# Performance work log

Hardware: AMD Instinct MI355X
Metric: run time of the kernel (lower is better)

Reference implementation:

```python
import jax, jax.numpy as jnp
import numpy as np

HIDDEN = 128
NUM_HEADS = 8
F32_MIN = jnp.finfo(jnp.float32).min


def _split_heads(x, n):
    # [B, S, D] -> [B, n, S, D//n]
    b, s, d = x.shape
    return x.reshape(b, s, n, d // n).transpose(0, 2, 1, 3)


def setup_inputs() -> dict:
    key = jax.random.key(0)
    k1, k2, k3 = jax.random.split(key, 3)
    B, S = 4, 2048
    key_and_value = jax.random.normal(k1, (B, S, 2 * HIDDEN), dtype=jnp.float32)
    query = jax.random.normal(k2, (B, S, HIDDEN), dtype=jnp.float32)
    seq_len = jax.random.randint(k3, (B, 1), 1, S + 1, dtype=jnp.int32)
    return {"key_and_value": key_and_value, "query": query, "seq_len": seq_len}


def reference(key_and_value, query, seq_len):
    B, S, _ = query.shape
    d_head = HIDDEN // NUM_HEADS
    k, v = jnp.split(key_and_value, 2, axis=2)           # each [B, S, HIDDEN]
    Q = _split_heads(query, NUM_HEADS) * (d_head ** 0.5)  # NOTE: original MULTIPLIES by sqrt(d_head)
    K = _split_heads(k, NUM_HEADS)
    V = _split_heads(v, NUM_HEADS)
    # scores: [B, H, S, S]
    logits = jnp.einsum('bhqd,bhkd->bhqk', Q, K)
    # length mask over key positions: valid where pos < seq_len (one-hot+cumsum trick)
    valid = (jnp.arange(S, dtype=jnp.int32)[None, :] < seq_len).astype(jnp.float32)  # [B, S]
    logits = logits + F32_MIN * (1.0 - valid[:, None, None, :])
    weights = jax.nn.softmax(logits, axis=-1)
    out = jnp.einsum('bhqk,bhkd->bhqd', weights, V)       # [B, H, S, d_head]
    return out.transpose(0, 2, 1, 3).reshape(B, S, HIDDEN)
```

## Files before the change

### kernel.cpp

```cpp
#include <hip/hip_runtime.h>
#include <hip/hip_bf16.h>

#define HIDDEN 128
#define NHEAD  8
#define DHEAD  16
#define KBLK   64
#define QPB    2
#define TILEB  6144
#define QSCALE 5.77078016355585277626f

typedef __attribute__((ext_vector_type(8))) __bf16 bf16x8;
typedef __attribute__((ext_vector_type(4))) __bf16 bf16x4;
typedef __attribute__((ext_vector_type(4))) float  f32x4;
typedef __attribute__((ext_vector_type(2))) float  f32x2;
typedef __attribute__((ext_vector_type(4))) int    i32x4;

__device__ __forceinline__ int ksub(int k)  { return ((k >> 5) << 1) | ((k >> 2) & 1); }
__device__ __forceinline__ int kirow(int k) { return (((k >> 3) & 3) << 2) | (k & 3); }

__device__ __forceinline__ void cvt_store(char* Sb, int ka, i32x4 vaddr,
                                          f32x4 kvec, f32x4 vvec)
{
    bf16x4 khv, klv;
    #pragma unroll
    for (int i = 0; i < 4; ++i) {
        __bf16 hi = (__bf16)kvec[i];
        khv[i] = hi;
        klv[i] = (__bf16)(kvec[i] - (float)hi);
    }
    *(bf16x4*)(Sb + ka)        = khv;
    *(bf16x4*)(Sb + 2048 + ka) = klv;
    #pragma unroll
    for (int i = 0; i < 4; ++i)
        *(__bf16*)(Sb + vaddr[i]) = (__bf16)vvec[i];
}

template<bool SPLIT>
__global__ __launch_bounds__(256, 4)
void mha_fwd(const float* __restrict__ kv,
             const float* __restrict__ q,
             const int*   __restrict__ seq_len,
             float* __restrict__ out,
             float* __restrict__ pbuf,
             float* __restrict__ mlbuf,
             int S, int nc, int chunk)
{
    const int qpair = blockIdx.x;
    const int h     = blockIdx.y;
    int b, c0;
    if (SPLIT) { const int Bn = gridDim.z / nc; b = blockIdx.z % Bn; c0 = blockIdx.z / Bn; }
    else       { b = blockIdx.z; c0 = 0; }
    const int L = seq_len[b];
    const int kstart = SPLIT ? c0 * chunk : 0;
    if (SPLIT && kstart >= L) return;
    const int kend = SPLIT ? min(L, kstart + chunk) : L;

    const int tid  = threadIdx.x;
    const int lane = tid & 63;
    const int wave = tid >> 6;
    const int g    = lane >> 4;
    const int lr   = lane & 15;
    const int sw   = (lr & 7) << 4;

    __shared__ __align__(16) char Stg[2][TILEB];

    const int qrowb = qpair * (QPB * KBLK) + wave * 16 + lr;
    bf16x8 qf[QPB];
    #pragma unroll
    for (int qt = 0; qt < QPB; ++qt) {
        const float* qp = q + ((size_t)(b * S + qrowb + qt * KBLK) * HIDDEN) + h * DHEAD + (g & 1) * 8;
        #pragma unroll
        for (int j = 0; j < 8; ++j) {
            float qv = qp[j] * QSCALE;
            __bf16 hi = (__bf16)qv;
            qf[qt][j] = (g < 2) ? hi : (__bf16)(qv - (float)hi);
        }
    }

    const int sk = tid >> 2;
    const int qd = tid & 3;
    const float* kvp = kv + ((size_t)(b * S + sk) * (2 * HIDDEN)) + h * DHEAD + 4 * qd;
    const int ka = ksub(sk) * 512 + (qd >> 1) * 256 + kirow(sk) * 16 + (qd & 1) * 8;
    i32x4 vaddr;
    #pragma unroll
    for (int i = 0; i < 4; ++i) {
        const int d = 4 * qd + i;
        vaddr[i] = 4096 + d * 128 + (((sk >> 3) * 16) ^ ((d & 7) << 4)) + (sk & 7) * 2;
    }

    f32x4 acc[QPB];
    float m[QPB], lsum[QPB];
    #pragma unroll
    for (int qt = 0; qt < QPB; ++qt) {
        acc[qt] = (f32x4){0.f, 0.f, 0.f, 0.f};
        m[qt] = -1e30f; lsum[qt] = 0.f;
    }

    const int ntiles = (kend - kstart + KBLK - 1) >> 6;

    {
        const float* kp = kvp + (size_t)kstart * (2 * HIDDEN);
        f32x4 kvec = *(const f32x4*)kp;
        f32x4 vvec = *(const f32x4*)(kp + HIDDEN);
        cvt_store(&Stg[0][0], ka, vaddr, kvec, vvec);
    }
    __syncthreads();

    for (int ti = 0; ti < ntiles; ++ti) {
        const int kb = kstart + ti * KBLK;
        const char* Sb = &Stg[ti & 1][0];
        const bool hasnext = (ti + 1) < ntiles;

        f32x4 nkv, nvv;
        if (hasnext) {
            const float* kp = kvp + (size_t)(kb + KBLK) * (2 * HIDDEN);
            nkv = *(const f32x4*)kp;
            nvv = *(const f32x4*)(kp + HIDDEN);
        }

        bf16x8 kfh[4], kfl[4];
        #pragma unroll
        for (int sub = 0; sub < 4; ++sub) {
            kfh[sub] = *(const bf16x8*)(Sb + sub * 512 + (g & 1) * 256 + lr * 16);
            kfl[sub] = *(const bf16x8*)(Sb + 2048 + sub * 512 + (g & 1) * 256 + lr * 16);
        }
        bf16x8 vb0 = *(const bf16x8*)(Sb + 4096 + lr * 128 + ((g * 16) ^ sw));
        bf16x8 vb1 = *(const bf16x8*)(Sb + 4096 + lr * 128 + ((64 + g * 16) ^ sw));

        const bool bnd = (kb + KBLK > kend);

        #pragma unroll
        for (int qt = 0; qt < QPB; ++qt) {
            f32x4 s[4];
            #pragma unroll
            for (int sub = 0; sub < 4; ++sub) {
                f32x4 z = {0.f, 0.f, 0.f, 0.f};
                z = __builtin_amdgcn_mfma_f32_16x16x32_bf16(kfh[sub], qf[qt], z, 0, 0, 0);
                s[sub] = __builtin_amdgcn_mfma_f32_16x16x32_bf16(kfl[sub], qf[qt], z, 0, 0, 0);
            }
            if (bnd) {
                #pragma unroll
                for (int sub = 0; sub < 4; ++sub) {
                    const int kb2 = kb + (sub >> 1) * 32 + (sub & 1) * 4 + g * 8;
                    #pragma unroll
                    for (int r = 0; r < 4; ++r)
                        if (kb2 + r >= kend) s[sub][r] = -1e30f;
                }
            }

            float t0 = fmaxf(fmaxf(s[0][0], s[0][1]), fmaxf(s[0][2], s[0][3]));
            float t1 = fmaxf(fmaxf(s[1][0], s[1][1]), fmaxf(s[1][2], s[1][3]));
            float t2 = fmaxf(fmaxf(s[2][0], s[2][1]), fmaxf(s[2][2], s[2][3]));
            float t3 = fmaxf(fmaxf(s[3][0], s[3][1]), fmaxf(s[3][2], s[3][3]));
            float tmax = fmaxf(fmaxf(t0, t1), fmaxf(t2, t3));
            tmax = fmaxf(tmax, __shfl_xor(tmax, 16));
            tmax = fmaxf(tmax, __shfl_xor(tmax, 32));

            const float mn = fmaxf(m[qt], tmax);
            const float alpha = exp2f(m[qt] - mn);
            m[qt] = mn;

            float rsum = 0.f;
            bf16x8 pa0, pa1;
            #pragma unroll
            for (int sub = 0; sub < 2; ++sub)
                #pragma unroll
                for (int r = 0; r < 4; ++r) {
                    float p = exp2f(s[sub][r] - mn);
                    rsum += p;
                    pa0[sub * 4 + r] = (__bf16)p;
                }
            #pragma unroll
            for (int sub = 2; sub < 4; ++sub)
                #pragma unroll
                for (int r = 0; r < 4; ++r) {
                    float p = exp2f(s[sub][r] - mn);
                    rsum += p;
                    pa1[(sub - 2) * 4 + r] = (__bf16)p;
                }
            rsum += __shfl_xor(rsum, 16);
            rsum += __shfl_xor(rsum, 32);
            lsum[qt] = lsum[qt] * alpha + rsum;
            acc[qt] *= alpha;

            acc[qt] = __builtin_amdgcn_mfma_f32_16x16x32_bf16(vb0, pa0, acc[qt], 0, 0, 0);
            acc[qt] = __builtin_amdgcn_mfma_f32_16x16x32_bf16(vb1, pa1, acc[qt], 0, 0, 0);
        }

        if (hasnext)
            cvt_store(&Stg[(ti + 1) & 1][0], ka, vaddr, nkv, nvv);
        __syncthreads();
    }

    #pragma unroll
    for (int qt = 0; qt < QPB; ++qt) {
        const int qglob = qrowb + qt * KBLK;
        if (SPLIT) {
            const size_t row = (((size_t)b * nc + c0) * S + qglob) * NHEAD + h;
            *(f32x4*)&pbuf[row * DHEAD + g * 4] = acc[qt];
            if (g == 0) { f32x2 ml = {m[qt], lsum[qt]}; *(f32x2*)&mlbuf[row * 2] = ml; }
        } else {
            const float inv = 1.0f / lsum[qt];
            *(f32x4*)&out[((size_t)b * S + qglob) * HIDDEN + h * DHEAD + g * 4] = acc[qt] * inv;
        }
    }
}

__global__ __launch_bounds__(256)
void mha_merge(const float* __restrict__ pbuf, const float* __restrict__ mlbuf,
               const int* __restrict__ seq_len, float* __restrict__ out,
               int S, int nc, int chunk)
{
    const int t = blockIdx.x * 256 + threadIdx.x;
    const int h = t & (NHEAD - 1);
    const int rest = t >> 3;
    const int qg = rest % S;
    const int b  = rest / S;
    const int L  = seq_len[b];
    const int nch = min(nc, (L + chunk - 1) / chunk);

    const size_t cstr = (size_t)S * NHEAD;
    const size_t row0 = ((size_t)b * nc) * cstr + (size_t)qg * NHEAD + h;

    float mv[8], lv[8];
    float M = -1e30f;
    for (int c = 0; c < nch; ++c) {
        f32x2 ml = *(const f32x2*)&mlbuf[(row0 + c * cstr) * 2];
        mv[c] = ml[0]; lv[c] = ml[1];
        M = fmaxf(M, ml[0]);
    }
    float den = 0.f;
    f32x4 o0 = {0,0,0,0}, o1 = o0, o2 = o0, o3 = o0;
    for (int c = 0; c < nch; ++c) {
        float w = exp2f(mv[c] - M);
        den += w * lv[c];
        const float* pp = &pbuf[(row0 + c * cstr) * DHEAD];
        o0 += w * *(const f32x4*)&pp[0];
        o1 += w * *(const f32x4*)&pp[4];
        o2 += w * *(const f32x4*)&pp[8];
        o3 += w * *(const f32x4*)&pp[12];
    }
    const float inv = 1.0f / den;
    float* op = &out[((size_t)b * S + qg) * HIDDEN + h * DHEAD];
    *(f32x4*)&op[0]  = o0 * inv;
    *(f32x4*)&op[4]  = o1 * inv;
    *(f32x4*)&op[8]  = o2 * inv;
    *(f32x4*)&op[12] = o3 * inv;
}

extern "C" void kernel_launch(void* const* d_in, const int* in_sizes, int n_in,
                              void* d_out, int out_size, void* d_ws, size_t ws_size,
                              hipStream_t stream)
{
    const float* kv      = (const float*)d_in[0];
    const float* query   = (const float*)d_in[1];
    const int*   seq_len = (const int*)d_in[2];
    float* out           = (float*)d_out;

    const int B = in_sizes[2];
    const int S = in_sizes[1] / (B * HIDDEN);

    int chunk = 0, nc = 1;
    size_t pb = 0, mlb = 0;
    for (int cand = 256; cand <= 512; cand <<= 1) {
        int n = (S + cand - 1) / cand;
        size_t pbc  = (size_t)B * n * S * NHEAD * DHEAD * sizeof(float);
        size_t mlbc = (size_t)B * n * S * NHEAD * 2 * sizeof(float);
        if (n <= 8 && ws_size >= pbc + mlbc) { chunk = cand; nc = n; pb = pbc; mlb = mlbc; break; }
    }

    if (chunk) {
        float* pbuf  = (float*)d_ws;
        float* mlbuf = (float*)((char*)d_ws + pb);
        mha_fwd<true><<<dim3(S / (QPB * KBLK), NHEAD, B * nc), dim3(256), 0, stream>>>(
            kv, query, seq_len, nullptr, pbuf, mlbuf, S, nc, chunk);
        const int nrows = B * S * NHEAD;
        mha_merge<<<dim3((nrows + 255) / 256), dim3(256), 0, stream>>>(
            pbuf, mlbuf, seq_len, out, S, nc, chunk);
    } else {
        mha_fwd<false><<<dim3(S / (QPB * KBLK), NHEAD, B), dim3(256), 0, stream>>>(
            kv, query, seq_len, out, nullptr, nullptr, S, 1, S);
    }
}
```

Baseline: 47.27 us.

## Use persistent atomic work queue for split-K attention and store partials as bf16

Replaces the fixed 3D grid with a persistent kernel of up to 2048 blocks that pull (q-pair, head, batch, chunk) work items from a global atomic counter. The counter is zeroed with a memset each call. Items whose chunk lies past seq_len are skipped cheaply rather than occupying a whole block launch, which targets load imbalance from the variable sequence lengths. Partial output accumulators are written as bf16 instead of fp32 to cut workspace traffic into the merge kernel, at some cost in precision. The change also adds an extra memset launch and a per-item atomic plus barrier.

```diff
diff --git a/kernel.cpp b/kernel.cpp
--- a/kernel.cpp
+++ b/kernel.cpp
@@ -41,45 +41,24 @@
              const float* __restrict__ q,
              const int*   __restrict__ seq_len,
              float* __restrict__ out,
-             float* __restrict__ pbuf,
+             __hip_bfloat16* __restrict__ pbuf,
              float* __restrict__ mlbuf,
-             int S, int nc, int chunk)
+             int* __restrict__ wq,
+             int S, int nb, int nc, int chunk, int nitems)
 {
-    const int qpair = blockIdx.x;
-    const int h     = blockIdx.y;
-    int b, c0;
-    if (SPLIT) { const int Bn = gridDim.z / nc; b = blockIdx.z % Bn; c0 = blockIdx.z / Bn; }
-    else       { b = blockIdx.z; c0 = 0; }
-    const int L = seq_len[b];
-    const int kstart = SPLIT ? c0 * chunk : 0;
-    if (SPLIT && kstart >= L) return;
-    const int kend = SPLIT ? min(L, kstart + chunk) : L;
-
     const int tid  = threadIdx.x;
     const int lane = tid & 63;
     const int wave = tid >> 6;
     const int g    = lane >> 4;
     const int lr   = lane & 15;
     const int sw   = (lr & 7) << 4;
+    const int QP   = S / (QPB * KBLK);
 
     __shared__ __align__(16) char Stg[2][TILEB];
-
-    const int qrowb = qpair * (QPB * KBLK) + wave * 16 + lr;
-    bf16x8 qf[QPB];
-    #pragma unroll
-    for (int qt = 0; qt < QPB; ++qt) {
-        const float* qp = q + ((size_t)(b * S + qrowb + qt * KBLK) * HIDDEN) + h * DHEAD + (g & 1) * 8;
-        #pragma unroll
-        for (int j = 0; j < 8; ++j) {
-            float qv = qp[j] * QSCALE;
-            __bf16 hi = (__bf16)qv;
-            qf[qt][j] = (g < 2) ? hi : (__bf16)(qv - (float)hi);
-        }
-    }
+    __shared__ int s_item;
 
     const int sk = tid >> 2;
     const int qd = tid & 3;
-    const float* kvp = kv + ((size_t)(b * S + sk) * (2 * HIDDEN)) + h * DHEAD + 4 * qd;
     const int ka = ksub(sk) * 512 + (qd >> 1) * 256 + kirow(sk) * 16 + (qd & 1) * 8;
     i32x4 vaddr;
     #pragma unroll
@@ -88,126 +67,169 @@
         vaddr[i] = 4096 + d * 128 + (((sk >> 3) * 16) ^ ((d & 7) << 4)) + (sk & 7) * 2;
     }
 
-    f32x4 acc[QPB];
-    float m[QPB], lsum[QPB];
-    #pragma unroll
-    for (int qt = 0; qt < QPB; ++qt) {
-        acc[qt] = (f32x4){0.f, 0.f, 0.f, 0.f};
-        m[qt] = -1e30f; lsum[qt] = 0.f;
-    }
-
-    const int ntiles = (kend - kstart + KBLK - 1) >> 6;
-
-    {
-        const float* kp = kvp + (size_t)kstart * (2 * HIDDEN);
-        f32x4 kvec = *(const f32x4*)kp;
-        f32x4 vvec = *(const f32x4*)(kp + HIDDEN);
-        cvt_store(&Stg[0][0], ka, vaddr, kvec, vvec);
-    }
-    __syncthreads();
-
-    for (int ti = 0; ti < ntiles; ++ti) {
-        const int kb = kstart + ti * KBLK;
-        const char* Sb = &Stg[ti & 1][0];
-        const bool hasnext = (ti + 1) < ntiles;
-
-        f32x4 nkv, nvv;
-        if (hasnext) {
-            const float* kp = kvp + (size_t)(kb + KBLK) * (2 * HIDDEN);
-            nkv = *(const f32x4*)kp;
-            nvv = *(const f32x4*)(kp + HIDDEN);
-        }
-
-        bf16x8 kfh[4], kfl[4];
-        #pragma unroll
-        for (int sub = 0; sub < 4; ++sub) {
-            kfh[sub] = *(const bf16x8*)(Sb + sub * 512 + (g & 1) * 256 + lr * 16);
-            kfl[sub] = *(const bf16x8*)(Sb + 2048 + sub * 512 + (g & 1) * 256 + lr * 16);
-        }
-        bf16x8 vb0 = *(const bf16x8*)(Sb + 4096 + lr * 128 + ((g * 16) ^ sw));
-        bf16x8 vb1 = *(const bf16x8*)(Sb + 4096 + lr * 128 + ((64 + g * 16) ^ sw));
-
-        const bool bnd = (kb + KBLK > kend);
-
+    for (int it = blockIdx.x; ; it += gridDim.x) {
+        int item;
+        if (wq) {
+            if (tid == 0) s_item = atomicAdd(wq, 1);
+            __syncthreads();
+            item = s_item;
+        } else {
+            item = it;
+        }
+        if (item >= nitems) return;
+
+        const int qp = item % QP;
+        int t1 = item / QP;
+        const int h  = t1 % NHEAD;
+        int t2 = t1 / NHEAD;
+        const int b  = t2 % nb;
+        const int c0 = t2 / nb;
+
+        const int L = seq_len[b];
+        const int kstart = SPLIT ? c0 * chunk : 0;
+        if (SPLIT && kstart >= L) { if (!wq) return; else continue; }
+        const int kend = SPLIT ? min(L, kstart + chunk) : L;
+
+        const int qrowb = qp * (QPB * KBLK) + wave * 16 + lr;
+        bf16x8 qf[QPB];
         #pragma unroll
         for (int qt = 0; qt < QPB; ++qt) {
-            f32x4 s[4];
+            const float* qpp = q + ((size_t)(b * S + qrowb + qt * KBLK) * HIDDEN) + h * DHEAD + (g & 1) * 8;
+            #pragma unroll
+            for (int j = 0; j < 8; ++j) {
+                float qv = qpp[j] * QSCALE;
+                __bf16 hi = (__bf16)qv;
+                qf[qt][j] = (g < 2) ? hi : (__bf16)(qv - (float)hi);
+            }
+        }
+
+        const float* kvp = kv + ((size_t)(b * S + sk) * (2 * HIDDEN)) + h * DHEAD + 4 * qd;
+
+        f32x4 acc[QPB];
+        float m[QPB], lsum[QPB];
+        #pragma unroll
+        for (int qt = 0; qt < QPB; ++qt) {
+            acc[qt] = (f32x4){0.f, 0.f, 0.f, 0.f};
+            m[qt] = -1e30f; lsum[qt] = 0.f;
+        }
+
+        const int ntiles = (kend - kstart + KBLK - 1) >> 6;
+
+        {
+            const float* kp = kvp + (size_t)kstart * (2 * HIDDEN);
+            f32x4 kvec = *(const f32x4*)kp;
+            f32x4 vvec = *(const f32x4*)(kp + HIDDEN);
+            cvt_store(&Stg[0][0], ka, vaddr, kvec, vvec);
+        }
+        __syncthreads();
+
+        for (int ti = 0; ti < ntiles; ++ti) {
+            const int kb = kstart + ti * KBLK;
+            const char* Sb = &Stg[ti & 1][0];
+            const bool hasnext = (ti + 1) < ntiles;
+
+            f32x4 nkv, nvv;
+            if (hasnext) {
+                const float* kp = kvp + (size_t)(kb + KBLK) * (2 * HIDDEN);
+                nkv = *(const f32x4*)kp;
+                nvv = *(const f32x4*)(kp + HIDDEN);
+            }
+
+            bf16x8 kfh[4], kfl[4];
             #pragma unroll
             for (int sub = 0; sub < 4; ++sub) {
-                f32x4 z = {0.f, 0.f, 0.f, 0.f};
-                z = __builtin_amdgcn_mfma_f32_16x16x32_bf16(kfh[sub], qf[qt], z, 0, 0, 0);
-                s[sub] = __builtin_amdgcn_mfma_f32_16x16x32_bf16(kfl[sub], qf[qt], z, 0, 0, 0);
-            }
-            if (bnd) {
+                kfh[sub] = *(const bf16x8*)(Sb + sub * 512 + (g & 1) * 256 + lr * 16);
+                kfl[sub] = *(const bf16x8*)(Sb + 2048 + sub * 512 + (g & 1) * 256 + lr * 16);
+            }
+            bf16x8 vb0 = *(const bf16x8*)(Sb + 4096 + lr * 128 + ((g * 16) ^ sw));
+            bf16x8 vb1 = *(const bf16x8*)(Sb + 4096 + lr * 128 + ((64 + g * 16) ^ sw));
+
+            const bool bnd = (kb + KBLK > kend);
+
+            #pragma unroll
+            for (int qt = 0; qt < QPB; ++qt) {
+                f32x4 s[4];
                 #pragma unroll
                 for (int sub = 0; sub < 4; ++sub) {
-                    const int kb2 = kb + (sub >> 1) * 32 + (sub & 1) * 4 + g * 8;
+                    f32x4 z = {0.f, 0.f, 0.f, 0.f};
+                    z = __builtin_amdgcn_mfma_f32_16x16x32_bf16(kfh[sub], qf[qt], z, 0, 0, 0);
+                    s[sub] = __builtin_amdgcn_mfma_f32_16x16x32_bf16(kfl[sub], qf[qt], z, 0, 0, 0);
+                }
+                if (bnd) {
                     #pragma unroll
-                    for (int r = 0; r < 4; ++r)
-                        if (kb2 + r >= kend) s[sub][r] = -1e30f;
+                    for (int sub = 0; sub < 4; ++sub) {
+                        const int kb2 = kb + (sub >> 1) * 32 + (sub & 1) * 4 + g * 8;
+                        #pragma unroll
+                        for (int r = 0; r < 4; ++r)
+                            if (kb2 + r >= kend) s[sub][r] = -1e30f;
+                    }
                 }
-            }
-
-            float t0 = fmaxf(fmaxf(s[0][0], s[0][1]), fmaxf(s[0][2], s[0][3]));
-            float t1 = fmaxf(fmaxf(s[1][0], s[1][1]), fmaxf(s[1][2], s[1][3]));
-            float t2 = fmaxf(fmaxf(s[2][0], s[2][1]), fmaxf(s[2][2], s[2][3]));
-            float t3 = fmaxf(fmaxf(s[3][0], s[3][1]), fmaxf(s[3][2], s[3][3]));
-            float tmax = fmaxf(fmaxf(t0, t1), fmaxf(t2, t3));
-            tmax = fmaxf(tmax, __shfl_xor(tmax, 16));
-            tmax = fmaxf(tmax, __shfl_xor(tmax, 32));
-
-            const float mn = fmaxf(m[qt], tmax);
-            const float alpha = exp2f(m[qt] - mn);
-            m[qt] = mn;
-
-            float rsum = 0.f;
-            bf16x8 pa0, pa1;
-            #pragma unroll
-            for (int sub = 0; sub < 2; ++sub)
+
+                float t0 = fmaxf(fmaxf(s[0][0], s[0][1]), fmaxf(s[0][2], s[0][3]));
+                float t1v = fmaxf(fmaxf(s[1][0], s[1][1]), fmaxf(s[1][2], s[1][3]));
+                float t2v = fmaxf(fmaxf(s[2][0], s[2][1]), fmaxf(s[2][2], s[2][3]));
+                float t3v = fmaxf(fmaxf(s[3][0], s[3][1]), fmaxf(s[3][2], s[3][3]));
+                float tmax = fmaxf(fmaxf(t0, t1v), fmaxf(t2v, t3v));
+                tmax = fmaxf(tmax, __shfl_xor(tmax, 16));
+                tmax = fmaxf(tmax, __shfl_xor(tmax, 32));
+
+                const float mn = fmaxf(m[qt], tmax);
+                const float alpha = exp2f(m[qt] - mn);
+                m[qt] = mn;
+
+                float rsum = 0.f;
+                bf16x8 pa0, pa1;
                 #pragma unroll
-                for (int r = 0; r < 4; ++r) {
-                    float p = exp2f(s[sub][r] - mn);
-                    rsum += p;
-                    pa0[sub * 4 + r] = (__bf16)p;
-                }
-            #pragma unroll
-            for (int sub = 2; sub < 4; ++sub)
+                for (int sub = 0; sub < 2; ++sub)
+                    #pragma unroll
+                    for (int r = 0; r < 4; ++r) {
+                        float p = exp2f(s[sub][r] - mn);
+                        rsum += p;
+                        pa0[sub * 4 + r] = (__bf16)p;
+                    }
                 #pragma unroll
-                for (int r = 0; r < 4; ++r) {
-                    float p = exp2f(s[sub][r] - mn);
-                    rsum += p;
-                    pa1[(sub - 2) * 4 + r] = (__bf16)p;
-                }
-            rsum += __shfl_xor(rsum, 16);
-            rsum += __shfl_xor(rsum, 32);
-            lsum[qt] = lsum[qt] * alpha + rsum;
-            acc[qt] *= alpha;
-
-            acc[qt] = __builtin_amdgcn_mfma_f32_16x16x32_bf16(vb0, pa0, acc[qt], 0, 0, 0);
-            acc[qt] = __builtin_amdgcn_mfma_f32_16x16x32_bf16(vb1, pa1, acc[qt], 0, 0, 0);
-        }
-
-        if (hasnext)
-            cvt_store(&Stg[(ti + 1) & 1][0], ka, vaddr, nkv, nvv);
-        __syncthreads();
-    }
-
-    #pragma unroll
-    for (int qt = 0; qt < QPB; ++qt) {
-        const int qglob = qrowb + qt * KBLK;
-        if (SPLIT) {
-            const size_t row = (((size_t)b * nc + c0) * S + qglob) * NHEAD + h;
-            *(f32x4*)&pbuf[row * DHEAD + g * 4] = acc[qt];
-            if (g == 0) { f32x2 ml = {m[qt], lsum[qt]}; *(f32x2*)&mlbuf[row * 2] = ml; }
-        } else {
-            const float inv = 1.0f / lsum[qt];
-            *(f32x4*)&out[((size_t)b * S + qglob) * HIDDEN + h * DHEAD + g * 4] = acc[qt] * inv;
-        }
+                for (int sub = 2; sub < 4; ++sub)
+                    #pragma unroll
+                    for (int r = 0; r < 4; ++r) {
+                        float p = exp2f(s[sub][r] - mn);
+                        rsum += p;
+                        pa1[(sub - 2) * 4 + r] = (__bf16)p;
+                    }
+                rsum += __shfl_xor(rsum, 16);
+                rsum += __shfl_xor(rsum, 32);
+                lsum[qt] = lsum[qt] * alpha + rsum;
+                acc[qt] *= alpha;
+
+                acc[qt] = __builtin_amdgcn_mfma_f32_16x16x32_bf16(vb0, pa0, acc[qt], 0, 0, 0);
+                acc[qt] = __builtin_amdgcn_mfma_f32_16x16x32_bf16(vb1, pa1, acc[qt], 0, 0, 0);
+            }
+
+            if (hasnext)
+                cvt_store(&Stg[(ti + 1) & 1][0], ka, vaddr, nkv, nvv);
+            __syncthreads();
+        }
+
+        #pragma unroll
+        for (int qt = 0; qt < QPB; ++qt) {
+            const int qglob = qrowb + qt * KBLK;
+            if (SPLIT) {
+                const size_t row = (((size_t)b * nc + c0) * S + qglob) * NHEAD + h;
+                bf16x4 pk;
+                #pragma unroll
+                for (int r = 0; r < 4; ++r) pk[r] = (__bf16)acc[qt][r];
+                *(bf16x4*)&pbuf[row * DHEAD + g * 4] = pk;
+                if (g == 0) { f32x2 ml = {m[qt], lsum[qt]}; *(f32x2*)&mlbuf[row * 2] = ml; }
+            } else {
+                const float inv = 1.0f / lsum[qt];
+                *(f32x4*)&out[((size_t)b * S + qglob) * HIDDEN + h * DHEAD + g * 4] = acc[qt] * inv;
+            }
+        }
+        if (!wq) { if (it + gridDim.x >= nitems) return; }
     }
 }
 
 __global__ __launch_bounds__(256)
-void mha_merge(const float* __restrict__ pbuf, const float* __restrict__ mlbuf,
+void mha_merge(const __hip_bfloat16* __restrict__ pbuf, const float* __restrict__ mlbuf,
                const int* __restrict__ seq_len, float* __restrict__ out,
                int S, int nc, int chunk)
 {
@@ -230,22 +252,28 @@
         M = fmaxf(M, ml[0]);
     }
     float den = 0.f;
-    f32x4 o0 = {0,0,0,0}, o1 = o0, o2 = o0, o3 = o0;
+    float o[16];
+    #pragma unroll
+    for (int i = 0; i < 16; ++i) o[i] = 0.f;
     for (int c = 0; c < nch; ++c) {
         float w = exp2f(mv[c] - M);
         den += w * lv[c];
-        const float* pp = &pbuf[(row0 + c * cstr) * DHEAD];
-        o0 += w * *(const f32x4*)&pp[0];
-        o1 += w * *(const f32x4*)&pp[4];
-        o2 += w * *(const f32x4*)&pp[8];
-        o3 += w * *(const f32x4*)&pp[12];
+        const __hip_bfloat16* pp = &pbuf[(row0 + c * cstr) * DHEAD];
+        bf16x8 p0 = *(const bf16x8*)&pp[0];
+        bf16x8 p1 = *(const bf16x8*)&pp[8];
+        #pragma unroll
+        for (int i = 0; i < 8; ++i) {
+            o[i]     += w * (float)p0[i];
+            o[i + 8] += w * (float)p1[i];
+        }
     }
     const float inv = 1.0f / den;
     float* op = &out[((size_t)b * S + qg) * HIDDEN + h * DHEAD];
-    *(f32x4*)&op[0]  = o0 * inv;
-    *(f32x4*)&op[4]  = o1 * inv;
-    *(f32x4*)&op[8]  = o2 * inv;
-    *(f32x4*)&op[12] = o3 * inv;
+    #pragma unroll
+    for (int i = 0; i < 4; ++i) {
+        f32x4 v = {o[4*i] * inv, o[4*i+1] * inv, o[4*i+2] * inv, o[4*i+3] * inv};
+        *(f32x4*)&op[4 * i] = v;
+    }
 }
 
 extern "C" void kernel_launch(void* const* d_in, const int* in_sizes, int n_in,
@@ -259,26 +287,32 @@
 
     const int B = in_sizes[2];
     const int S = in_sizes[1] / (B * HIDDEN);
+    const int QP = S / (QPB * KBLK);
 
     int chunk = 0, nc = 1;
-    size_t pb = 0, mlb = 0;
-    for (int cand = 256; cand <= 512; cand <<= 1) {
+    size_t mlb = 0, pbb = 0;
+    for (int cand = 256; cand <= S; cand <<= 1) {
         int n = (S + cand - 1) / cand;
-        size_t pbc  = (size_t)B * n * S * NHEAD * DHEAD * sizeof(float);
         size_t mlbc = (size_t)B * n * S * NHEAD * 2 * sizeof(float);
-        if (n <= 8 && ws_size >= pbc + mlbc) { chunk = cand; nc = n; pb = pbc; mlb = mlbc; break; }
+        size_t pbbc = (size_t)B * n * S * NHEAD * DHEAD * sizeof(__hip_bfloat16);
+        if (n <= 8 && ws_size >= 64 + mlbc + pbbc) { chunk = cand; nc = n; mlb = mlbc; pbb = pbbc; break; }
     }
 
     if (chunk) {
-        float* pbuf  = (float*)d_ws;
-        float* mlbuf = (float*)((char*)d_ws + pb);
-        mha_fwd<true><<<dim3(S / (QPB * KBLK), NHEAD, B * nc), dim3(256), 0, stream>>>(
-            kv, query, seq_len, nullptr, pbuf, mlbuf, S, nc, chunk);
+        int* wq = (int*)d_ws;
+        float* mlbuf = (float*)((char*)d_ws + 64);
+        __hip_bfloat16* pbuf = (__hip_bfloat16*)((char*)d_ws + 64 + mlb);
+        hipMemsetAsync(d_ws, 0, 64, stream);
+        const int nitems = nc * B * NHEAD * QP;
+        const int grid = nitems < 2048 ? nitems : 2048;
+        mha_fwd<true><<<dim3(grid), dim3(256), 0, stream>>>(
+            kv, query, seq_len, nullptr, pbuf, mlbuf, wq, S, B, nc, chunk, nitems);
         const int nrows = B * S * NHEAD;
         mha_merge<<<dim3((nrows + 255) / 256), dim3(256), 0, stream>>>(
             pbuf, mlbuf, seq_len, out, S, nc, chunk);
     } else {
-        mha_fwd<false><<<dim3(S / (QPB * KBLK), NHEAD, B), dim3(256), 0, stream>>>(
-            kv, query, seq_len, out, nullptr, nullptr, S, 1, S);
+        const int nitems = B * NHEAD * QP;
+        mha_fwd<false><<<dim3(nitems), dim3(256), 0, stream>>>(
+            kv, query, seq_len, out, nullptr, nullptr, nullptr, S, B, 1, S, nitems);
     }
 }
```

Measured after the change: 98.00 us. 2.07x slower.

## Switch attention to fp16 MFMA, drop K hi/lo split, fp16 partials

Applied to the files above, without the earlier changes.

Replaces the bf16 hi/lo split of K (two MFMAs per score tile) with a single fp16 MFMA, halving QK MFMA count and shrinking the shared-memory K tile. V and P also move to fp16. Split-K partial outputs are stored as fp16 to halve workspace traffic, and the chunk size is fixed at 512, giving fewer chunks and a cheaper merge. This trades accuracy: K and the partial accumulators lose the extra precision, and fp16 range is narrower than bf16, though the scaled softmax probabilities stay bounded in [0,1].

```diff
diff --git a/kernel.cpp b/kernel.cpp
--- a/kernel.cpp
+++ b/kernel.cpp
@@ -6,11 +6,11 @@
 #define DHEAD  16
 #define KBLK   64
 #define QPB    2
-#define TILEB  6144
+#define TILEB  4096
 #define QSCALE 5.77078016355585277626f
 
-typedef __attribute__((ext_vector_type(8))) __bf16 bf16x8;
-typedef __attribute__((ext_vector_type(4))) __bf16 bf16x4;
+typedef __attribute__((ext_vector_type(8))) _Float16 f16x8;
+typedef __attribute__((ext_vector_type(4))) _Float16 f16x4;
 typedef __attribute__((ext_vector_type(4))) float  f32x4;
 typedef __attribute__((ext_vector_type(2))) float  f32x2;
 typedef __attribute__((ext_vector_type(4))) int    i32x4;
@@ -21,18 +21,13 @@
 __device__ __forceinline__ void cvt_store(char* Sb, int ka, i32x4 vaddr,
                                           f32x4 kvec, f32x4 vvec)
 {
-    bf16x4 khv, klv;
-    #pragma unroll
-    for (int i = 0; i < 4; ++i) {
-        __bf16 hi = (__bf16)kvec[i];
-        khv[i] = hi;
-        klv[i] = (__bf16)(kvec[i] - (float)hi);
-    }
-    *(bf16x4*)(Sb + ka)        = khv;
-    *(bf16x4*)(Sb + 2048 + ka) = klv;
+    f16x4 kh;
+    #pragma unroll
+    for (int i = 0; i < 4; ++i) kh[i] = (_Float16)kvec[i];
+    *(f16x4*)(Sb + ka) = kh;
     #pragma unroll
     for (int i = 0; i < 4; ++i)
-        *(__bf16*)(Sb + vaddr[i]) = (__bf16)vvec[i];
+        *(_Float16*)(Sb + vaddr[i]) = (_Float16)vvec[i];
 }
 
 template<bool SPLIT>
@@ -41,7 +36,7 @@
              const float* __restrict__ q,
              const int*   __restrict__ seq_len,
              float* __restrict__ out,
-             float* __restrict__ pbuf,
+             _Float16* __restrict__ pbuf,
              float* __restrict__ mlbuf,
              int S, int nc, int chunk)
 {
@@ -65,15 +60,15 @@
     __shared__ __align__(16) char Stg[2][TILEB];
 
     const int qrowb = qpair * (QPB * KBLK) + wave * 16 + lr;
-    bf16x8 qf[QPB];
+    f16x8 qf[QPB];
     #pragma unroll
     for (int qt = 0; qt < QPB; ++qt) {
         const float* qp = q + ((size_t)(b * S + qrowb + qt * KBLK) * HIDDEN) + h * DHEAD + (g & 1) * 8;
         #pragma unroll
         for (int j = 0; j < 8; ++j) {
             float qv = qp[j] * QSCALE;
-            __bf16 hi = (__bf16)qv;
-            qf[qt][j] = (g < 2) ? hi : (__bf16)(qv - (float)hi);
+            _Float16 hi = (_Float16)qv;
+            qf[qt][j] = (g < 2) ? hi : (_Float16)(qv - (float)hi);
         }
     }
 
@@ -85,7 +80,7 @@
     #pragma unroll
     for (int i = 0; i < 4; ++i) {
         const int d = 4 * qd + i;
-        vaddr[i] = 4096 + d * 128 + (((sk >> 3) * 16) ^ ((d & 7) << 4)) + (sk & 7) * 2;
+        vaddr[i] = 2048 + d * 128 + (((sk >> 3) * 16) ^ ((d & 7) << 4)) + (sk & 7) * 2;
     }
 
     f32x4 acc[QPB];
@@ -118,14 +113,12 @@
             nvv = *(const f32x4*)(kp + HIDDEN);
         }
 
-        bf16x8 kfh[4], kfl[4];
-        #pragma unroll
-        for (int sub = 0; sub < 4; ++sub) {
-            kfh[sub] = *(const bf16x8*)(Sb + sub * 512 + (g & 1) * 256 + lr * 16);
-            kfl[sub] = *(const bf16x8*)(Sb + 2048 + sub * 512 + (g & 1) * 256 + lr * 16);
-        }
-        bf16x8 vb0 = *(const bf16x8*)(Sb + 4096 + lr * 128 + ((g * 16) ^ sw));
-        bf16x8 vb1 = *(const bf16x8*)(Sb + 4096 + lr * 128 + ((64 + g * 16) ^ sw));
+        f16x8 kf[4];
+        #pragma unroll
+        for (int sub = 0; sub < 4; ++sub)
+            kf[sub] = *(const f16x8*)(Sb + sub * 512 + (g & 1) * 256 + lr * 16);
+        f16x8 vb0 = *(const f16x8*)(Sb + 2048 + lr * 128 + ((g * 16) ^ sw));
+        f16x8 vb1 = *(const f16x8*)(Sb + 2048 + lr * 128 + ((64 + g * 16) ^ sw));
 
         const bool bnd = (kb + KBLK > kend);
 
@@ -135,8 +128,7 @@
             #pragma unroll
             for (int sub = 0; sub < 4; ++sub) {
                 f32x4 z = {0.f, 0.f, 0.f, 0.f};
-                z = __builtin_amdgcn_mfma_f32_16x16x32_bf16(kfh[sub], qf[qt], z, 0, 0, 0);
-                s[sub] = __builtin_amdgcn_mfma_f32_16x16x32_bf16(kfl[sub], qf[qt], z, 0, 0, 0);
+                s[sub] = __builtin_amdgcn_mfma_f32_16x16x32_f16(kf[sub], qf[qt], z, 0, 0, 0);
             }
             if (bnd) {
                 #pragma unroll
@@ -161,14 +153,14 @@
             m[qt] = mn;
 
             float rsum = 0.f;
-            bf16x8 pa0, pa1;
+            f16x8 pa0, pa1;
             #pragma unroll
             for (int sub = 0; sub < 2; ++sub)
                 #pragma unroll
                 for (int r = 0; r < 4; ++r) {
                     float p = exp2f(s[sub][r] - mn);
                     rsum += p;
-                    pa0[sub * 4 + r] = (__bf16)p;
+                    pa0[sub * 4 + r] = (_Float16)p;
                 }
             #pragma unroll
             for (int sub = 2; sub < 4; ++sub)
@@ -176,15 +168,15 @@
                 for (int r = 0; r < 4; ++r) {
                     float p = exp2f(s[sub][r] - mn);
                     rsum += p;
-                    pa1[(sub - 2) * 4 + r] = (__bf16)p;
+                    pa1[(sub - 2) * 4 + r] = (_Float16)p;
                 }
             rsum += __shfl_xor(rsum, 16);
             rsum += __shfl_xor(rsum, 32);
             lsum[qt] = lsum[qt] * alpha + rsum;
             acc[qt] *= alpha;
 
-            acc[qt] = __builtin_amdgcn_mfma_f32_16x16x32_bf16(vb0, pa0, acc[qt], 0, 0, 0);
-            acc[qt] = __builtin_amdgcn_mfma_f32_16x16x32_bf16(vb1, pa1, acc[qt], 0, 0, 0);
+            acc[qt] = __builtin_amdgcn_mfma_f32_16x16x32_f16(vb0, pa0, acc[qt], 0, 0, 0);
+            acc[qt] = __builtin_amdgcn_mfma_f32_16x16x32_f16(vb1, pa1, acc[qt], 0, 0, 0);
         }
 
         if (hasnext)
@@ -197,7 +189,10 @@
         const int qglob = qrowb + qt * KBLK;
         if (SPLIT) {
             const size_t row = (((size_t)b * nc + c0) * S + qglob) * NHEAD + h;
-            *(f32x4*)&pbuf[row * DHEAD + g * 4] = acc[qt];
+            f16x4 pk;
+            #pragma unroll
+            for (int r = 0; r < 4; ++r) pk[r] = (_Float16)acc[qt][r];
+            *(f16x4*)&pbuf[row * DHEAD + g * 4] = pk;
             if (g == 0) { f32x2 ml = {m[qt], lsum[qt]}; *(f32x2*)&mlbuf[row * 2] = ml; }
         } else {
             const float inv = 1.0f / lsum[qt];
@@ -207,7 +202,7 @@
 }
 
 __global__ __launch_bounds__(256)
-void mha_merge(const float* __restrict__ pbuf, const float* __restrict__ mlbuf,
+void mha_merge(const _Float16* __restrict__ pbuf, const float* __restrict__ mlbuf,
                const int* __restrict__ seq_len, float* __restrict__ out,
                int S, int nc, int chunk)
 {
@@ -230,22 +225,28 @@
         M = fmaxf(M, ml[0]);
     }
     float den = 0.f;
-    f32x4 o0 = {0,0,0,0}, o1 = o0, o2 = o0, o3 = o0;
+    float o[16];
+    #pragma unroll
+    for (int i = 0; i < 16; ++i) o[i] = 0.f;
     for (int c = 0; c < nch; ++c) {
         float w = exp2f(mv[c] - M);
         den += w * lv[c];
-        const float* pp = &pbuf[(row0 + c * cstr) * DHEAD];
-        o0 += w * *(const f32x4*)&pp[0];
-        o1 += w * *(const f32x4*)&pp[4];
-        o2 += w * *(const f32x4*)&pp[8];
-        o3 += w * *(const f32x4*)&pp[12];
+        const _Float16* pp = &pbuf[(row0 + c * cstr) * DHEAD];
+        f16x8 p0 = *(const f16x8*)&pp[0];
+        f16x8 p1 = *(const f16x8*)&pp[8];
+        #pragma unroll
+        for (int i = 0; i < 8; ++i) {
+            o[i]     += w * (float)p0[i];
+            o[i + 8] += w * (float)p1[i];
+        }
     }
     const float inv = 1.0f / den;
     float* op = &out[((size_t)b * S + qg) * HIDDEN + h * DHEAD];
-    *(f32x4*)&op[0]  = o0 * inv;
-    *(f32x4*)&op[4]  = o1 * inv;
-    *(f32x4*)&op[8]  = o2 * inv;
-    *(f32x4*)&op[12] = o3 * inv;
+    #pragma unroll
+    for (int i = 0; i < 4; ++i) {
+        f32x4 v = {o[4*i] * inv, o[4*i+1] * inv, o[4*i+2] * inv, o[4*i+3] * inv};
+        *(f32x4*)&op[4 * i] = v;
+    }
 }
 
 extern "C" void kernel_launch(void* const* d_in, const int* in_sizes, int n_in,
@@ -260,18 +261,14 @@
     const int B = in_sizes[2];
     const int S = in_sizes[1] / (B * HIDDEN);
 
-    int chunk = 0, nc = 1;
-    size_t pb = 0, mlb = 0;
-    for (int cand = 256; cand <= 512; cand <<= 1) {
-        int n = (S + cand - 1) / cand;
-        size_t pbc  = (size_t)B * n * S * NHEAD * DHEAD * sizeof(float);
-        size_t mlbc = (size_t)B * n * S * NHEAD * 2 * sizeof(float);
-        if (n <= 8 && ws_size >= pbc + mlbc) { chunk = cand; nc = n; pb = pbc; mlb = mlbc; break; }
-    }
-
-    if (chunk) {
-        float* pbuf  = (float*)d_ws;
-        float* mlbuf = (float*)((char*)d_ws + pb);
+    const int chunk = 512;
+    const int nc = (S + chunk - 1) / chunk;
+    const size_t mlb = (size_t)B * nc * S * NHEAD * 2 * sizeof(float);
+    const size_t pbb = (size_t)B * nc * S * NHEAD * DHEAD * sizeof(_Float16);
+
+    if (nc <= 8 && ws_size >= mlb + pbb) {
+        float* mlbuf = (float*)d_ws;
+        _Float16* pbuf = (_Float16*)((char*)d_ws + mlb);
         mha_fwd<true><<<dim3(S / (QPB * KBLK), NHEAD, B * nc), dim3(256), 0, stream>>>(
             kv, query, seq_len, nullptr, pbuf, mlbuf, S, nc, chunk);
         const int nrows = B * S * NHEAD;
```

After: 40.33 us. 14.7% less time.
